# Kernel tuning notes

Measured on AMD Instinct MI355X. Metric: run time of the kernel, lower is better.

## Reference

```python
import jax, jax.numpy as jnp
import numpy as np
import math

N = 100000       # nodes
E = 640000       # edges
VOCAB = 8192
EMB = 96         # node_embedding_dim
SEL = 32         # node_selector_dim
H = EMB + SEL    # hidden_dim = 128
T = 3            # num_edge_types
P = 64           # positional_embedding_dim
MAXPOS = 512     # max_edge_position
ITERS = 6        # ggnn_iterations


def _sinusoidal(max_pos, dim):
    pos = np.arange(max_pos)[:, None].astype(np.float32)
    div = np.exp(np.arange(0, dim, 2).astype(np.float32) * (-math.log(10000.0) / dim))
    pe = np.zeros((max_pos, dim), np.float32)
    pe[:, 0::2] = np.sin(pos * div)
    pe[:, 1::2] = np.cos(pos * div)
    return jnp.asarray(pe)


def setup_inputs() -> dict:
    key = jax.random.key(0)
    ks = jax.random.split(key, 20)
    s = 1.0 / np.sqrt(H).astype(np.float32)
    inp = {
        "x_text_indices": jax.random.randint(ks[0], (N,), 0, VOCAB, dtype=jnp.int32),
        "node_selectors": jax.random.normal(ks[1], (N, SEL), jnp.float32),
        "edge_index": jax.random.randint(ks[2], (2, E), 0, N, dtype=jnp.int32),
        "edge_type": jax.random.randint(ks[3], (E,), 0, T, dtype=jnp.int32),
        "edge_positions": jax.random.randint(ks[4], (E,), 0, MAXPOS + 1, dtype=jnp.int32),
        "emb": (jax.random.normal(ks[5], (VOCAB, EMB), jnp.float32) * 0.02).at[0].set(0.0),  # padding_idx=0
        "pos_enc": _sinusoidal(MAXPOS + 1, P),
        "Wg": jax.random.normal(ks[6], (P, H), jnp.float32) * (1.0 / np.sqrt(P)),
        "bg": jnp.zeros((H,), jnp.float32),
        "Wt": jax.random.normal(ks[7], (T, H, H), jnp.float32) * s,
        "bt": jnp.zeros((T, H), jnp.float32),
        "W_ih": jax.random.normal(ks[8], (3 * H, H), jnp.float32) * s,
        "W_hh": jax.random.normal(ks[9], (3 * H, H), jnp.float32) * s,
        "b_ih": jnp.zeros((3 * H,), jnp.float32),
        "b_hh": jnp.zeros((3 * H,), jnp.float32),
        "W1": jax.random.normal(ks[10], (2 * H, H), jnp.float32) * (1.0 / np.sqrt(2 * H)),
        "b1": jnp.zeros((H,), jnp.float32),
        "W2": jax.random.normal(ks[11], (H, 1), jnp.float32) * s,
        "b2": jnp.zeros((1,), jnp.float32),
    }
    return inp


def _gru_cell(x, h, W_ih, W_hh, b_ih, b_hh):
    # torch.nn.GRUCell math
    gi = x @ W_ih.T + b_ih          # [N, 3H]
    gh = h @ W_hh.T + b_hh          # [N, 3H]
    i_r, i_z, i_n = jnp.split(gi, 3, axis=-1)
    h_r, h_z, h_n = jnp.split(gh, 3, axis=-1)
    r = jax.nn.sigmoid(i_r + h_r)
    z = jax.nn.sigmoid(i_z + h_z)
    n = jnp.tanh(i_n + r * h_n)
    return (1.0 - z) * n + z * h


def reference(x_text_indices, node_selectors, edge_index, edge_type, edge_positions,
              emb, pos_enc, Wg, bg, Wt, bt, W_ih, W_hh, b_ih, b_hh, W1, b1, W2, b2):
    src, dst = edge_index[0], edge_index[1]
    h0 = jnp.concatenate([emb[x_text_indices], node_selectors], axis=-1)  # [N, H]
    pe_e = pos_enc[edge_positions]                                        # [E, P]
    gate = 2.0 * jax.nn.sigmoid(pe_e @ Wg + bg)                           # [E, H]
    cnt = jax.ops.segment_sum(jnp.ones((E,), h0.dtype), dst, num_segments=N)
    denom = jnp.maximum(cnt, 1.0)[:, None]                                # mean-scatter, 0 if no in-edges

    h = h0
    for _ in range(ITERS):
        gx = h[src] * gate                                                # gather + gate [E, H]
        # edge-type routed linear: sum over the one active type per edge
        msg = jnp.zeros_like(gx)
        for t in range(T):
            mask = (edge_type == t)[:, None].astype(gx.dtype)
            msg = msg + mask * (gx @ Wt[t] + bt[t])
        agg = jax.ops.segment_sum(msg, dst, num_segments=N) / denom       # mean aggregation [N, H]
        h = _gru_cell(agg, h, W_ih, W_hh, b_ih, b_hh)

    feats = jnp.concatenate([h, h0], axis=-1)                             # [N, 2H]
    logits = jax.nn.relu(feats @ W1 + b1) @ W2 + b2                       # [N, 1]
    return logits
```

## Files before the change

### kernel.cpp

```cpp
#include <hip/hip_runtime.h>
#include <cstdint>
#include <cstddef>

#define HD 128
#define EMBD 96
#define SELD 32
#define PD 64
#define NPOS 513
#define GITERS 6

typedef _Float16 f16;
typedef __attribute__((ext_vector_type(8))) _Float16 f16x8;
typedef __attribute__((ext_vector_type(4))) _Float16 f16x4;
typedef __attribute__((ext_vector_type(2))) _Float16 f16x2;
typedef __attribute__((ext_vector_type(4))) float f32x4;

__device__ __forceinline__ float sigm(float x) {
    return __builtin_amdgcn_rcpf(1.0f + __expf(-x));
}
__device__ __forceinline__ float tanh_f(float x) {
    return 2.0f * __builtin_amdgcn_rcpf(1.0f + __expf(-2.0f * x)) - 1.0f;
}


__global__ void k_deg(const int* __restrict__ ei, const int* __restrict__ et,
                      int* __restrict__ cnt_t, int E, int N) {
    int e = blockIdx.x * 256 + threadIdx.x;
    if (e < E) {
        int d = ei[E + e];
        atomicAdd(&cnt_t[(size_t)et[e] * N + d], 1);
    }
}

__launch_bounds__(1024)
__global__ void k_scan1(const int* __restrict__ cnt_t, int* __restrict__ rp,
                        int* __restrict__ bsum, int N) {
    __shared__ int sc[1024];
    int t = threadIdx.x;
    int i = blockIdx.x * 1024 + t;
    int v = 0;
    if (i < N)
        v = cnt_t[i] + cnt_t[(size_t)N + i] + cnt_t[2 * (size_t)N + i];
    sc[t] = v;
    __syncthreads();
    for (int off = 1; off < 1024; off <<= 1) {
        int u = (t >= off) ? sc[t - off] : 0;
        __syncthreads();
        sc[t] += u;
        __syncthreads();
    }
    if (i < N) rp[i] = sc[t] - v;
    if (t == 1023) bsum[blockIdx.x] = sc[t];
}

__launch_bounds__(1024)
__global__ void k_scan2(int* __restrict__ bsum, int nb) {
    __shared__ int sc[1024];
    int t = threadIdx.x;
    int v = (t < nb) ? bsum[t] : 0;
    sc[t] = v;
    __syncthreads();
    for (int off = 1; off < 1024; off <<= 1) {
        int u = (t >= off) ? sc[t - off] : 0;
        __syncthreads();
        sc[t] += u;
        __syncthreads();
    }
    if (t < nb) bsum[t] = sc[t] - v;
}

__global__ void k_scan3(const int* __restrict__ rp, const int* __restrict__ bsum,
                        const int* __restrict__ cnt_t, float4* __restrict__ cntp,
                        int4* __restrict__ rp4, int N) {
    int i = blockIdx.x * 256 + threadIdx.x;
    if (i < N) {
        int start = rp[i] + bsum[i >> 10];
        int c0 = cnt_t[i];
        int c1 = cnt_t[(size_t)N + i];
        int c2 = cnt_t[2 * (size_t)N + i];
        rp4[i] = make_int4(start, start + c0, start + c0 + c1, start + c0 + c1 + c2);
        float4 v;
        v.x = (float)c0; v.y = (float)c1; v.z = (float)c2;
        v.w = 1.0f / fmaxf((float)(c0 + c1 + c2), 1.0f);
        cntp[i] = v;
    }
}

__global__ void k_fill(const int* __restrict__ ei, const int* __restrict__ et,
                       const int* __restrict__ ep, const int4* __restrict__ rp4,
                       int* __restrict__ cur3, int2* __restrict__ e2, int E, int N) {
    int e = blockIdx.x * 256 + threadIdx.x;
    if (e < E) {
        int d = ei[E + e];
        int t = et[e];
        int4 r4 = rp4[d];
        int base = (t == 0) ? r4.x : ((t == 1) ? r4.y : r4.z);
        int pos = atomicAdd(&cur3[(size_t)t * N + d], 1);
        e2[base + pos] = make_int2(ei[e], ep[e]);
    }
}

__global__ void k_gate(const float* __restrict__ pe, const float* __restrict__ Wg,
                       const float* __restrict__ bg, f16* __restrict__ gb) {
    int p = blockIdx.x;
    int j = threadIdx.x;
    float acc = bg[j];
    #pragma unroll 8
    for (int k = 0; k < PD; ++k) acc += pe[p * PD + k] * Wg[k * HD + j];
    gb[p * HD + j] = (f16)(2.0f * sigm(acc));
}

__global__ void k_prep(const float* __restrict__ Wt, const float* __restrict__ W1,
                       f16* __restrict__ WtT, f16* __restrict__ W1T) {
    const int SZ = 3 * HD * HD;
    int id = blockIdx.x * 256 + threadIdx.x;
    if (id < SZ) {
        int t = id / (HD * HD), rem = id % (HD * HD);
        int n = rem / HD, k = rem % HD;
        WtT[id] = (f16)Wt[t * HD * HD + k * HD + n];
    } else if (id < SZ + 2 * HD * HD) {
        int rem = id - SZ;
        int n = rem / (2 * HD), k = rem % (2 * HD);
        W1T[rem] = (f16)W1[k * HD + n];
    }
}

__global__ void k_prepW(const float* __restrict__ Wih, const float* __restrict__ Whh,
                        f16* __restrict__ Wcat) {
    int id = blockIdx.x * 256 + threadIdx.x;
    if (id < 512 * 256) {
        int j = id >> 8, k = id & 255;
        float v;
        if (j < 256)      v = (k < 128) ? Wih[j * 128 + k] : Whh[j * 128 + (k - 128)];
        else if (j < 384) v = (k < 128) ? Wih[j * 128 + k] : 0.0f;
        else              v = (k < 128) ? 0.0f : Whh[(j - 128) * 128 + (k - 128)];
        Wcat[id] = (f16)v;
    }
}

__global__ void k_init(const int* __restrict__ xidx, const float* __restrict__ sel,
                       const float* __restrict__ emb, f16* __restrict__ h, int N) {
    int id = blockIdx.x * 256 + threadIdx.x;
    if (id < N * HD) {
        int n = id >> 7, j = id & 127;
        float v = (j < EMBD) ? emb[(size_t)xidx[n] * EMBD + j]
                             : sel[(size_t)n * SELD + (j - EMBD)];
        h[id] = (f16)v;
    }
}

__launch_bounds__(256, 6)
__global__ void k_agg(const int4* __restrict__ rp4, const int2* __restrict__ e2,
                      const f16* __restrict__ h_in, const f16* __restrict__ gb,
                      const f16* __restrict__ WtT, const float* __restrict__ bt,
                      const float4* __restrict__ cntp, f16* __restrict__ agg, int N) {
    __shared__ f16 S[3 * 16 * 136];
    __shared__ f16 aggL[16 * 136];

    int tid = threadIdx.x;
    int wave = tid >> 6, lane = tid & 63;
    int quad = lane >> 4, m = lane & 15;
    int qw = lane >> 4, ql = lane & 15;
    int d0 = blockIdx.x * 16;

    {
        int lrow = wave * 4 + qw;
        int grow = d0 + lrow;
        bool valid = grow < N;
        int4 r4 = rp4[min(grow, N - 1)];
        int es = r4.x, b1 = r4.y, b2 = r4.z, ee = r4.w;
        if (!valid) ee = es;
        int dg = ee - es;
        int t1 = max(dg, __shfl_xor(dg, 16));
        int t2 = max(t1, __shfl_xor(t1, 32));
        int nb = (__builtin_amdgcn_readfirstlane(t2) + 3) >> 2;
        int co = ql * 8;

        const f16x8 zf = {0, 0, 0, 0, 0, 0, 0, 0};
        f16x8 accA = zf, accB = zf, accC = zf;
        for (int b = 0; b < nb; ++b) {
            int e0 = es + b * 4;
            int2 ev[4];
            #pragma unroll
            for (int j = 0; j < 4; ++j) {
                int idx = max(min(e0 + j, ee - 1), 0);
                ev[j] = e2[idx];
            }
            f16x8 hv[4], gv[4];
            #pragma unroll
            for (int j = 0; j < 4; ++j) {
                hv[j] = *(const f16x8*)(h_in + (size_t)ev[j].x * HD + co);
                gv[j] = *(const f16x8*)(gb + (size_t)ev[j].y * HD + co);
            }
            #pragma unroll
            for (int j = 0; j < 4; ++j) {
                int eidx = e0 + j;
                f16x8 g0 = (eidx < ee) ? gv[j] : zf;
                accA += hv[j] * g0;
                f16x8 gB = (eidx >= b1) ? g0 : zf;
                accB += hv[j] * gB;
                f16x8 gC = (eidx >= b2) ? g0 : zf;
                accC += hv[j] * gC;
            }
        }
        f16x8 s0 = accA - accB;
        f16x8 s1 = accB - accC;
        *(f16x8*)(S + (0 * 16 + lrow) * 136 + co) = s0;
        *(f16x8*)(S + (1 * 16 + lrow) * 136 + co) = s1;
        *(f16x8*)(S + (2 * 16 + lrow) * 136 + co) = accC;
    }
    __syncthreads();

    #pragma unroll
    for (int s = 0; s < 2; ++s) {
        int col = (wave + s * 4) * 16 + m;
        f32x4 acc = {0.f, 0.f, 0.f, 0.f};
        #pragma unroll
        for (int t = 0; t < 3; ++t)
            #pragma unroll
            for (int c = 0; c < 4; ++c) {
                f16x8 a = *(const f16x8*)(S + (t * 16 + m) * 136 + c * 32 + quad * 8);
                f16x8 b = *(const f16x8*)(WtT + ((size_t)t * HD + col) * HD + c * 32 + quad * 8);
                acc = __builtin_amdgcn_mfma_f32_16x16x32_f16(a, b, acc, 0, 0, 0);
            }
        float bt0 = bt[col], bt1 = bt[HD + col], bt2 = bt[2 * HD + col];
        #pragma unroll
        for (int r = 0; r < 4; ++r) {
            int lr = quad * 4 + r;
            int dd2 = min(d0 + lr, N - 1);
            float4 cp = cntp[dd2];
            float v = (acc[r] + cp.x * bt0 + cp.y * bt1 + cp.z * bt2) * cp.w;
            aggL[lr * 136 + col] = (f16)v;
        }
    }
    __syncthreads();

    {
        int row = tid >> 4, ch = tid & 15;
        if (d0 + row < N) {
            f16x8 v = *(const f16x8*)(aggL + row * 136 + ch * 8);
            *(f16x8*)(agg + (size_t)(d0 + row) * HD + ch * 8) = v;
        }
    }
}

__launch_bounds__(512, 2)
__global__ void k_gru(const f16* __restrict__ agg, const f16* __restrict__ h_in,
                      const f16* __restrict__ Wcat, const float* __restrict__ bih,
                      const float* __restrict__ bhh, f16* __restrict__ h_out, int N) {
    __shared__ f16 AL[64 * 264];

    int tid = threadIdx.x;
    int wave = tid >> 6, lane = tid & 63;
    int quad = lane >> 4, m = lane & 15;
    int j = wave * 16 + m;

    f16x8 br[8], bz[8], bn[8];
    #pragma unroll
    for (int c = 0; c < 8; ++c) {
        br[c] = *(const f16x8*)(Wcat + (size_t)j * 256 + c * 32 + quad * 8);
        bz[c] = *(const f16x8*)(Wcat + (size_t)(128 + j) * 256 + c * 32 + quad * 8);
        bn[c] = (c < 4)
            ? *(const f16x8*)(Wcat + (size_t)(256 + j) * 256 + c * 32 + quad * 8)
            : *(const f16x8*)(Wcat + (size_t)(384 + j) * 256 + c * 32 + quad * 8);
    }
    float b_r  = bih[j] + bhh[j];
    float b_z  = bih[HD + j] + bhh[HD + j];
    float b_in = bih[2 * HD + j];
    float b_hn = bhh[2 * HD + j];

    for (int t = 0; t < 4; ++t) {
        int d0 = blockIdx.x * 256 + t * 64;
        if (d0 >= N) break;

        __syncthreads();

        {
            int rsub = tid >> 5;
            int ch = tid & 31;
            #pragma unroll
            for (int i = 0; i < 4; ++i) {
                int row = i * 16 + rsub;
                int grow = min(d0 + row, N - 1);
                f16x8 v = (ch < 16)
                    ? *(const f16x8*)(agg + (size_t)grow * HD + ch * 8)
                    : *(const f16x8*)(h_in + (size_t)grow * HD + (ch - 16) * 8);
                *(f16x8*)(AL + row * 264 + ch * 8) = v;
            }
        }
        __syncthreads();

        float hp[4][4];
        #pragma unroll
        for (int tp = 0; tp < 2; ++tp) {
            f32x4 ar[2], az[2], an[2], ah[2];
            const f32x4 z4 = {0.f, 0.f, 0.f, 0.f};
            ar[0] = z4; ar[1] = z4; az[0] = z4; az[1] = z4;
            an[0] = z4; an[1] = z4; ah[0] = z4; ah[1] = z4;

            #pragma unroll
            for (int c = 0; c < 8; ++c) {
                #pragma unroll
                for (int t2 = 0; t2 < 2; ++t2) {
                    int tau = tp * 2 + t2;
                    f16x8 a = *(const f16x8*)(AL + (tau * 16 + m) * 264 + c * 32 + quad * 8);
                    ar[t2] = __builtin_amdgcn_mfma_f32_16x16x32_f16(a, br[c], ar[t2], 0, 0, 0);
                    az[t2] = __builtin_amdgcn_mfma_f32_16x16x32_f16(a, bz[c], az[t2], 0, 0, 0);
                    if (c < 4) an[t2] = __builtin_amdgcn_mfma_f32_16x16x32_f16(a, bn[c], an[t2], 0, 0, 0);
                    else       ah[t2] = __builtin_amdgcn_mfma_f32_16x16x32_f16(a, bn[c], ah[t2], 0, 0, 0);
                }
            }
            #pragma unroll
            for (int t2 = 0; t2 < 2; ++t2)
                #pragma unroll
                for (int r = 0; r < 4; ++r) {
                    int row = (tp * 2 + t2) * 16 + quad * 4 + r;
                    float hval = (float)AL[row * 264 + 128 + j];
                    float rr = sigm(ar[t2][r] + b_r);
                    float zz = sigm(az[t2][r] + b_z);
                    float nn = tanh_f(an[t2][r] + b_in + rr * (ah[t2][r] + b_hn));
                    hp[tp * 2 + t2][r] = (1.0f - zz) * nn + zz * hval;
                }
        }
        __syncthreads();

        #pragma unroll
        for (int tau = 0; tau < 4; ++tau)
            #pragma unroll
            for (int r = 0; r < 4; ++r)
                AL[(tau * 16 + quad * 4 + r) * 132 + j] = (f16)hp[tau][r];
        __syncthreads();

        {
            int rsub = tid >> 5, ch = tid & 31;
            #pragma unroll
            for (int i = 0; i < 4; ++i) {
                int row = i * 16 + rsub;
                if (d0 + row < N) {
                    f16x4 v = *(const f16x4*)(AL + row * 132 + ch * 4);
                    *(f16x4*)(h_out + (size_t)(d0 + row) * HD + ch * 4) = v;
                }
            }
        }
    }
}

__launch_bounds__(256)
__global__ void k_final(const f16* __restrict__ h_f, const int* __restrict__ xidx,
                        const float* __restrict__ sel, const float* __restrict__ emb,
                        const f16* __restrict__ W1T, const float* __restrict__ b1,
                        const float* __restrict__ W2, const float* __restrict__ b2,
                        float* __restrict__ out, int N) {
    __shared__ float red[4][16];
    int tid = threadIdx.x;
    int wave = tid >> 6, lane = tid & 63;
    int quad = lane >> 4, m = lane & 15;
    int row0 = blockIdx.x * 16;
    int arow = min(row0 + m, N - 1);
    int xi = xidx[arow];

    f16x8 fa[8];
    #pragma unroll
    for (int c = 0; c < 4; ++c)
        fa[c] = *(const f16x8*)(h_f + (size_t)arow * HD + c * 32 + quad * 8);
    #pragma unroll
    for (int c = 4; c < 7; ++c) {
        const float* ep = emb + (size_t)xi * EMBD + (c - 4) * 32 + quad * 8;
        #pragma unroll
        for (int jj = 0; jj < 8; ++jj) fa[c][jj] = (f16)ep[jj];
    }
    {
        const float* sp = sel + (size_t)arow * SELD + quad * 8;
        #pragma unroll
        for (int jj = 0; jj < 8; ++jj) fa[7][jj] = (f16)sp[jj];
    }

    f32x4 acc[2];
    const f32x4 z4 = {0.f, 0.f, 0.f, 0.f};
    acc[0] = z4; acc[1] = z4;
    #pragma unroll
    for (int s = 0; s < 2; ++s) {
        int c0 = (wave * 2 + s) * 16;
        #pragma unroll
        for (int c = 0; c < 8; ++c) {
            f16x8 b = *(const f16x8*)(W1T + (size_t)(c0 + m) * (2 * HD) + c * 32 + quad * 8);
            acc[s] = __builtin_amdgcn_mfma_f32_16x16x32_f16(fa[c], b, acc[s], 0, 0, 0);
        }
    }

    float psum[4] = {0.f, 0.f, 0.f, 0.f};
    #pragma unroll
    for (int s = 0; s < 2; ++s) {
        int col = (wave * 2 + s) * 16 + m;
        float b1v = b1[col], w2v = W2[col];
        #pragma unroll
        for (int r = 0; r < 4; ++r)
            psum[r] += fmaxf(acc[s][r] + b1v, 0.0f) * w2v;
    }
    #pragma unroll
    for (int off = 1; off < 16; off <<= 1)
        #pragma unroll
        for (int r = 0; r < 4; ++r) psum[r] += __shfl_xor(psum[r], off);

    if (m == 0) {
        #pragma unroll
        for (int r = 0; r < 4; ++r) red[wave][quad * 4 + r] = psum[r];
    }
    __syncthreads();
    if (tid < 16) {
        int row = row0 + tid;
        if (row < N) out[row] = red[0][tid] + red[1][tid] + red[2][tid] + red[3][tid] + b2[0];
    }
}


extern "C" void kernel_launch(void* const* d_in, const int* in_sizes, int n_in,
                              void* d_out, int out_size, void* d_ws, size_t ws_size,
                              hipStream_t stream) {
    const int*   xidx = (const int*)d_in[0];
    const float* sel  = (const float*)d_in[1];
    const int*   ei   = (const int*)d_in[2];
    const int*   et   = (const int*)d_in[3];
    const int*   ep   = (const int*)d_in[4];
    const float* emb  = (const float*)d_in[5];
    const float* pe   = (const float*)d_in[6];
    const float* Wg   = (const float*)d_in[7];
    const float* bg   = (const float*)d_in[8];
    const float* Wt   = (const float*)d_in[9];
    const float* bt   = (const float*)d_in[10];
    const float* Wih  = (const float*)d_in[11];
    const float* Whh  = (const float*)d_in[12];
    const float* bih  = (const float*)d_in[13];
    const float* bhh  = (const float*)d_in[14];
    const float* W1   = (const float*)d_in[15];
    const float* b1   = (const float*)d_in[16];
    const float* W2   = (const float*)d_in[17];
    const float* b2   = (const float*)d_in[18];

    const int N = in_sizes[0];
    const int E = in_sizes[3];
    const size_t NH = (size_t)N * HD;

    char* p = (char*)d_ws;
    f16*    hbf0  = (f16*)p;    p += NH * 2;
    f16*    hbf1  = (f16*)p;    p += NH * 2;
    f16*    aggb  = (f16*)p;    p += NH * 2;
    f16*    gb    = (f16*)p;    p += (size_t)NPOS * HD * 2;
    f16*    WtT   = (f16*)p;    p += 3 * HD * HD * 2;
    f16*    Wcat  = (f16*)p;    p += 512 * 256 * 2;
    f16*    W1T   = (f16*)p;    p += 2 * HD * HD * 2;
    float4* cntp  = (float4*)p; p += (size_t)N * 16;
    int4*   rp4   = (int4*)p;   p += (size_t)N * 16;
    int* cnt_t  = (int*)p; p += 3 * (size_t)N * 4;
    int* rp     = (int*)p; p += (size_t)N * 4;
    int* cur3   = (int*)p; p += 3 * (size_t)N * 4;
    int* bsum   = (int*)p; p += 1024 * 4;
    int2* e2    = (int2*)p;

    hipMemsetAsync(cnt_t, 0, 3 * (size_t)N * sizeof(int), stream);
    hipMemsetAsync(cur3, 0, 3 * (size_t)N * sizeof(int), stream);
    k_deg<<<(E + 255) / 256, 256, 0, stream>>>(ei, et, cnt_t, E, N);
    const int nb1 = (N + 1023) / 1024;
    k_scan1<<<nb1, 1024, 0, stream>>>(cnt_t, rp, bsum, N);
    k_scan2<<<1, 1024, 0, stream>>>(bsum, nb1);
    k_scan3<<<(N + 255) / 256, 256, 0, stream>>>(rp, bsum, cnt_t, cntp, rp4, N);
    k_fill<<<(E + 255) / 256, 256, 0, stream>>>(ei, et, ep, rp4, cur3, e2, E, N);
    k_gate<<<NPOS, HD, 0, stream>>>(pe, Wg, bg, gb);
    k_prep<<<(3 * HD * HD + 2 * HD * HD + 255) / 256, 256, 0, stream>>>(Wt, W1, WtT, W1T);
    k_prepW<<<512, 256, 0, stream>>>(Wih, Whh, Wcat);
    k_init<<<(N * HD + 255) / 256, 256, 0, stream>>>(xidx, sel, emb, hbf0, N);

    const int gA = (N + 15) / 16;
    const int gG = (N + 255) / 256;
    const f16* hin = hbf0;
    f16* hout = hbf1;
    for (int it = 0; it < GITERS; ++it) {
        k_agg<<<gA, 256, 0, stream>>>(rp4, e2, hin, gb, WtT, bt, cntp, aggb, N);
        k_gru<<<gG, 512, 0, stream>>>(aggb, hin, Wcat, bih, bhh, hout, N);
        const f16* tmp = hout;
        hout = (f16*)hin;
        hin = tmp;
    }

    const int gF = (N + 15) / 16;
    k_final<<<gF, 256, 0, stream>>>(hin, xidx, sel, emb, W1T, b1, W2, b2, (float*)d_out, N);
}
```

Measured before the change: 1.208 ms.

## Renumber nodes by in-degree to balance per-block aggregation work

Computes each node's in-degree, buckets nodes by degree (capped at 63) and renumbers them so nodes with similar degree sit next to each other. The CSR, the hidden state and the edge sources all use the new numbering, and final outputs are scattered back through new2old. The aim is to even out the work of the 16-node blocks in the aggregation kernel and cut wave divergence. In exchange it adds several small preprocessing kernels and extra atomics, and it scatters gathers of source rows, which may hurt locality. The two weight-prep kernels are also merged into one, and the memsets are combined into one.

```diff
diff --git a/kernel.cpp b/kernel.cpp
--- a/kernel.cpp
+++ b/kernel.cpp
@@ -23,12 +23,47 @@
 }
 
 
-__global__ void k_deg(const int* __restrict__ ei, const int* __restrict__ et,
-                      int* __restrict__ cnt_t, int E, int N) {
+__global__ void k_deg1(const int* __restrict__ ei, int* __restrict__ deg, int E) {
+    int e = blockIdx.x * 256 + threadIdx.x;
+    if (e < E) atomicAdd(&deg[ei[E + e]], 1);
+}
+
+__global__ void k_hist(const int* __restrict__ deg, int* __restrict__ hist, int N) {
+    int i = blockIdx.x * 256 + threadIdx.x;
+    if (i < N) atomicAdd(&hist[min(deg[i], 63)], 1);
+}
+
+__global__ void k_hscan(const int* __restrict__ hist, int* __restrict__ hbase) {
+    int t = threadIdx.x;
+    int v = hist[t];
+    int s = v;
+    for (int off = 1; off < 64; off <<= 1) {
+        int u = __shfl_up(s, off);
+        if (t >= off) s += u;
+    }
+    hbase[t] = s - v;
+}
+
+__global__ void k_rank(const int* __restrict__ deg, const int* __restrict__ hbase,
+                       int* __restrict__ hcur, int* __restrict__ old2new,
+                       int* __restrict__ new2old, int N) {
+    int i = blockIdx.x * 256 + threadIdx.x;
+    if (i < N) {
+        int b = min(deg[i], 63);
+        int r = atomicAdd(&hcur[b], 1);
+        int nid = hbase[b] + r;
+        old2new[i] = nid;
+        new2old[nid] = i;
+    }
+}
+
+__global__ void k_cnt2(const int* __restrict__ ei, const int* __restrict__ et,
+                       const int* __restrict__ old2new, int* __restrict__ cnt_t,
+                       int E, int N) {
     int e = blockIdx.x * 256 + threadIdx.x;
     if (e < E) {
-        int d = ei[E + e];
-        atomicAdd(&cnt_t[(size_t)et[e] * N + d], 1);
+        int nd = old2new[ei[E + e]];
+        atomicAdd(&cnt_t[(size_t)et[e] * N + nd], 1);
     }
 }
 
@@ -88,15 +123,17 @@
 
 __global__ void k_fill(const int* __restrict__ ei, const int* __restrict__ et,
                        const int* __restrict__ ep, const int4* __restrict__ rp4,
-                       int* __restrict__ cur3, int2* __restrict__ e2, int E, int N) {
+                       const int* __restrict__ old2new, int* __restrict__ cur3,
+                       int2* __restrict__ e2, int E, int N) {
     int e = blockIdx.x * 256 + threadIdx.x;
     if (e < E) {
-        int d = ei[E + e];
+        int nd = old2new[ei[E + e]];
+        int ns = old2new[ei[e]];
         int t = et[e];
-        int4 r4 = rp4[d];
+        int4 r4 = rp4[nd];
         int base = (t == 0) ? r4.x : ((t == 1) ? r4.y : r4.z);
-        int pos = atomicAdd(&cur3[(size_t)t * N + d], 1);
-        e2[base + pos] = make_int2(ei[e], ep[e]);
+        int pos = atomicAdd(&cur3[(size_t)t * N + nd], 1);
+        e2[base + pos] = make_int2(ns, ep[e]);
     }
 }
 
@@ -110,41 +147,41 @@
     gb[p * HD + j] = (f16)(2.0f * sigm(acc));
 }
 
-__global__ void k_prep(const float* __restrict__ Wt, const float* __restrict__ W1,
-                       f16* __restrict__ WtT, f16* __restrict__ W1T) {
+__global__ void k_prepM(const float* __restrict__ Wt, const float* __restrict__ W1,
+                        const float* __restrict__ Wih, const float* __restrict__ Whh,
+                        f16* __restrict__ WtT, f16* __restrict__ W1T,
+                        f16* __restrict__ Wcat) {
     const int SZ = 3 * HD * HD;
+    const int SZ2 = SZ + 2 * HD * HD;
     int id = blockIdx.x * 256 + threadIdx.x;
     if (id < SZ) {
         int t = id / (HD * HD), rem = id % (HD * HD);
         int n = rem / HD, k = rem % HD;
         WtT[id] = (f16)Wt[t * HD * HD + k * HD + n];
-    } else if (id < SZ + 2 * HD * HD) {
+    } else if (id < SZ2) {
         int rem = id - SZ;
         int n = rem / (2 * HD), k = rem % (2 * HD);
         W1T[rem] = (f16)W1[k * HD + n];
-    }
-}
-
-__global__ void k_prepW(const float* __restrict__ Wih, const float* __restrict__ Whh,
-                        f16* __restrict__ Wcat) {
-    int id = blockIdx.x * 256 + threadIdx.x;
-    if (id < 512 * 256) {
-        int j = id >> 8, k = id & 255;
+    } else if (id < SZ2 + 512 * 256) {
+        int rem = id - SZ2;
+        int j = rem >> 8, k = rem & 255;
         float v;
         if (j < 256)      v = (k < 128) ? Wih[j * 128 + k] : Whh[j * 128 + (k - 128)];
         else if (j < 384) v = (k < 128) ? Wih[j * 128 + k] : 0.0f;
         else              v = (k < 128) ? 0.0f : Whh[(j - 128) * 128 + (k - 128)];
-        Wcat[id] = (f16)v;
+        Wcat[rem] = (f16)v;
     }
 }
 
 __global__ void k_init(const int* __restrict__ xidx, const float* __restrict__ sel,
-                       const float* __restrict__ emb, f16* __restrict__ h, int N) {
+                       const float* __restrict__ emb, const int* __restrict__ new2old,
+                       f16* __restrict__ h, int N) {
     int id = blockIdx.x * 256 + threadIdx.x;
     if (id < N * HD) {
-        int n = id >> 7, j = id & 127;
-        float v = (j < EMBD) ? emb[(size_t)xidx[n] * EMBD + j]
-                             : sel[(size_t)n * SELD + (j - EMBD)];
+        int r = id >> 7, j = id & 127;
+        int orig = new2old[r];
+        float v = (j < EMBD) ? emb[(size_t)xidx[orig] * EMBD + j]
+                             : sel[(size_t)orig * SELD + (j - EMBD)];
         h[id] = (f16)v;
     }
 }
@@ -348,6 +385,7 @@
 __launch_bounds__(256)
 __global__ void k_final(const f16* __restrict__ h_f, const int* __restrict__ xidx,
                         const float* __restrict__ sel, const float* __restrict__ emb,
+                        const int* __restrict__ new2old,
                         const f16* __restrict__ W1T, const float* __restrict__ b1,
                         const float* __restrict__ W2, const float* __restrict__ b2,
                         float* __restrict__ out, int N) {
@@ -357,7 +395,8 @@
     int quad = lane >> 4, m = lane & 15;
     int row0 = blockIdx.x * 16;
     int arow = min(row0 + m, N - 1);
-    int xi = xidx[arow];
+    int orig = new2old[arow];
+    int xi = xidx[orig];
 
     f16x8 fa[8];
     #pragma unroll
@@ -370,7 +409,7 @@
         for (int jj = 0; jj < 8; ++jj) fa[c][jj] = (f16)ep[jj];
     }
     {
-        const float* sp = sel + (size_t)arow * SELD + quad * 8;
+        const float* sp = sel + (size_t)orig * SELD + quad * 8;
         #pragma unroll
         for (int jj = 0; jj < 8; ++jj) fa[7][jj] = (f16)sp[jj];
     }
@@ -409,7 +448,8 @@
     __syncthreads();
     if (tid < 16) {
         int row = row0 + tid;
-        if (row < N) out[row] = red[0][tid] + red[1][tid] + red[2][tid] + red[3][tid] + b2[0];
+        if (row < N)
+            out[new2old[row]] = red[0][tid] + red[1][tid] + red[2][tid] + red[3][tid] + b2[0];
     }
 }
 
@@ -451,24 +491,35 @@
     f16*    W1T   = (f16*)p;    p += 2 * HD * HD * 2;
     float4* cntp  = (float4*)p; p += (size_t)N * 16;
     int4*   rp4   = (int4*)p;   p += (size_t)N * 16;
-    int* cnt_t  = (int*)p; p += 3 * (size_t)N * 4;
-    int* rp     = (int*)p; p += (size_t)N * 4;
-    int* cur3   = (int*)p; p += 3 * (size_t)N * 4;
-    int* bsum   = (int*)p; p += 1024 * 4;
-    int2* e2    = (int2*)p;
-
-    hipMemsetAsync(cnt_t, 0, 3 * (size_t)N * sizeof(int), stream);
-    hipMemsetAsync(cur3, 0, 3 * (size_t)N * sizeof(int), stream);
-    k_deg<<<(E + 255) / 256, 256, 0, stream>>>(ei, et, cnt_t, E, N);
+    int* zbase  = (int*)p;
+    int* deg    = zbase;                 p += (size_t)N * 4;
+    int* cnt_t  = (int*)p;               p += 3 * (size_t)N * 4;
+    int* cur3   = (int*)p;               p += 3 * (size_t)N * 4;
+    int* hist   = (int*)p;               p += 64 * 4;
+    int* hcur   = (int*)p;               p += 64 * 4;
+    const size_t zbytes = (7 * (size_t)N + 128) * 4;
+    int* hbase   = (int*)p;              p += 64 * 4;
+    int* rp      = (int*)p;              p += (size_t)N * 4;
+    int* bsum    = (int*)p;              p += 1024 * 4;
+    int* old2new = (int*)p;              p += (size_t)N * 4;
+    int* new2old = (int*)p;              p += (size_t)N * 4;
+    int2* e2     = (int2*)p;
+
+    hipMemsetAsync(zbase, 0, zbytes, stream);
+    k_deg1<<<(E + 255) / 256, 256, 0, stream>>>(ei, deg, E);
+    k_hist<<<(N + 255) / 256, 256, 0, stream>>>(deg, hist, N);
+    k_hscan<<<1, 64, 0, stream>>>(hist, hbase);
+    k_rank<<<(N + 255) / 256, 256, 0, stream>>>(deg, hbase, hcur, old2new, new2old, N);
+    k_cnt2<<<(E + 255) / 256, 256, 0, stream>>>(ei, et, old2new, cnt_t, E, N);
     const int nb1 = (N + 1023) / 1024;
     k_scan1<<<nb1, 1024, 0, stream>>>(cnt_t, rp, bsum, N);
     k_scan2<<<1, 1024, 0, stream>>>(bsum, nb1);
     k_scan3<<<(N + 255) / 256, 256, 0, stream>>>(rp, bsum, cnt_t, cntp, rp4, N);
-    k_fill<<<(E + 255) / 256, 256, 0, stream>>>(ei, et, ep, rp4, cur3, e2, E, N);
+    k_fill<<<(E + 255) / 256, 256, 0, stream>>>(ei, et, ep, rp4, old2new, cur3, e2, E, N);
     k_gate<<<NPOS, HD, 0, stream>>>(pe, Wg, bg, gb);
-    k_prep<<<(3 * HD * HD + 2 * HD * HD + 255) / 256, 256, 0, stream>>>(Wt, W1, WtT, W1T);
-    k_prepW<<<512, 256, 0, stream>>>(Wih, Whh, Wcat);
-    k_init<<<(N * HD + 255) / 256, 256, 0, stream>>>(xidx, sel, emb, hbf0, N);
+    k_prepM<<<(3 * HD * HD + 2 * HD * HD + 512 * 256 + 255) / 256, 256, 0, stream>>>(
+        Wt, W1, Wih, Whh, WtT, W1T, Wcat);
+    k_init<<<(N * HD + 255) / 256, 256, 0, stream>>>(xidx, sel, emb, new2old, hbf0, N);
 
     const int gA = (N + 15) / 16;
     const int gG = (N + 255) / 256;
@@ -483,5 +534,6 @@
     }
 
     const int gF = (N + 15) / 16;
-    k_final<<<gF, 256, 0, stream>>>(hin, xidx, sel, emb, W1T, b1, W2, b2, (float*)d_out, N);
-}
+    k_final<<<gF, 256, 0, stream>>>(hin, xidx, sel, emb, new2old, W1T, b1, W2, b2,
+                                    (float*)d_out, N);
+}
```

New measurement: 1.941 ms. 60.8% more time.
